# Performance work log

Hardware: AMD Instinct MI355X
Metric: run time of the kernel (lower is better)

Reference implementation:

```python
import jax, jax.numpy as jnp
import numpy as np

DIM = 512
HEADS = 8
DIM_HEAD = DIM // 8          # 64
M_LAND = DIM // 2            # 256 landmarks
PINV_ITERS = 6
KS = 33                      # residual depthwise conv kernel
EPS = 1e-8
LN_EPS = 1e-5


def setup_inputs() -> dict:
    key = jax.random.key(0)
    ks = jax.random.split(key, 5)
    b, n = 2, 8192
    inner = HEADS * DIM_HEAD
    x = jax.random.normal(ks[0], (b, n, DIM), jnp.float32)
    mask = jnp.ones((b, n), jnp.bool_)
    w_qkv = jax.random.normal(ks[1], (DIM, 3 * inner), jnp.float32) / np.sqrt(DIM)
    w_out = jax.random.normal(ks[2], (inner, DIM), jnp.float32) / np.sqrt(inner)
    b_out = jnp.zeros((DIM,), jnp.float32)
    conv_w = jax.random.normal(ks[3], (HEADS, 1, KS, 1), jnp.float32) / np.sqrt(KS)
    ln_w = jnp.ones((DIM,), jnp.float32)
    ln_b = jnp.zeros((DIM,), jnp.float32)
    return dict(x=x, mask=mask, ln_w=ln_w, ln_b=ln_b,
                w_qkv=w_qkv, w_out=w_out, b_out=b_out, conv_w=conv_w)


def _moore_penrose_pinv(x, iters):
    # lucidrains iterative pinv: z0 = x^T / (max(col_sums) * max(row_sums))
    abs_x = jnp.abs(x)
    col = abs_x.sum(-1)
    row = abs_x.sum(-2)
    z = jnp.swapaxes(x, -1, -2) / (jnp.max(col) * jnp.max(row))
    I = jnp.eye(x.shape[-1], dtype=x.dtype)
    for _ in range(iters):
        xz = x @ z
        z = 0.25 * z @ (13 * I - xz @ (15 * I - xz @ (7 * I - xz)))
    return z


def reference(x, mask, ln_w, ln_b, w_qkv, w_out, b_out, conv_w):
    b, n, _ = x.shape
    # LayerNorm (pre-norm)
    mu = x.mean(-1, keepdims=True)
    var = ((x - mu) ** 2).mean(-1, keepdims=True)
    xn = (x - mu) / jnp.sqrt(var + LN_EPS) * ln_w + ln_b
    # front-pad seq to multiple of num_landmarks (static; no-op when divisible)
    pad = (M_LAND - n % M_LAND) % M_LAND
    if pad:
        xn = jnp.pad(xn, ((0, 0), (pad, 0), (0, 0)))
        mask = jnp.pad(mask, ((0, 0), (pad, 0)), constant_values=False)
    N = n + pad
    qkv = xn @ w_qkv
    q, k, v = jnp.split(qkv, 3, axis=-1)
    rs = lambda t: t.reshape(b, N, HEADS, DIM_HEAD).transpose(0, 2, 1, 3)  # b h N d
    q, k, v = rs(q), rs(k), rs(v)
    m3 = mask[:, None, :]                       # b 1 N
    mf = m3[..., None].astype(q.dtype)
    q, k, v = q * mf, k * mf, v * mf
    q = q * (DIM_HEAD ** -0.5)
    l = N // M_LAND                             # tokens per landmark
    ql = q.reshape(b, HEADS, M_LAND, l, DIM_HEAD).sum(3)
    kl = k.reshape(b, HEADS, M_LAND, l, DIM_HEAD).sum(3)
    m_land_sum = m3.astype(q.dtype).reshape(b, 1, M_LAND, l).sum(-1)   # b 1 M
    divisor = m_land_sum[..., None] + EPS
    ql = ql / divisor
    kl = kl / divisor
    m_land = m_land_sum > 0                     # b 1 M
    sim1 = jnp.einsum('bhid,bhjd->bhij', q, kl)    # b h N M
    sim2 = jnp.einsum('bhid,bhjd->bhij', ql, kl)   # b h M M
    sim3 = jnp.einsum('bhid,bhjd->bhij', ql, k)    # b h M N
    NEG = -jnp.finfo(q.dtype).max
    sim1 = jnp.where(m3[..., None] & m_land[..., None, :], sim1, NEG)
    sim2 = jnp.where(m_land[..., None] & m_land[..., None, :], sim2, NEG)
    sim3 = jnp.where(m_land[..., None] & m3[..., None, :], sim3, NEG)
    a1 = jax.nn.softmax(sim1, -1)
    a2 = jax.nn.softmax(sim2, -1)
    a3 = jax.nn.softmax(sim3, -1)
    a2_inv = _moore_penrose_pinv(a2, PINV_ITERS)
    out = (a1 @ a2_inv) @ (a3 @ v)              # b h N d
    # residual depthwise conv over sequence dim (per head)
    res = jax.lax.conv_general_dilated(
        v, conv_w, window_strides=(1, 1),
        padding=((KS // 2, KS // 2), (0, 0)),
        dimension_numbers=('NCHW', 'OIHW', 'NCHW'),
        feature_group_count=HEADS)
    out = out + res
    out = out.transpose(0, 2, 1, 3).reshape(b, N, HEADS * DIM_HEAD)
    out = out @ w_out + b_out                   # dropout is identity at eval
    out = out[:, -n:]
    return x + out
```

## Files before the change

### kernel.cpp

```cpp
#include <hip/hip_runtime.h>


typedef __attribute__((ext_vector_type(8))) short bf16x8;
typedef __attribute__((ext_vector_type(4))) float f32x4;

static __device__ __forceinline__ ushort f2bf(float f) {
  union { float f; unsigned u; } c; c.f = f;
  const unsigned r = c.u + 0x7fffu + ((c.u >> 16) & 1u);
  return (ushort)(r >> 16);
}
static __device__ __forceinline__ float bf2f(ushort u) {
  union { unsigned u; float f; } c; c.u = ((unsigned)u) << 16;
  return c.f;
}

typedef __attribute__((address_space(1))) const unsigned int guint;
typedef __attribute__((address_space(3))) unsigned int luint;
static __device__ __forceinline__ void gload_lds16(const void* g, void* l) {
  __builtin_amdgcn_global_load_lds((guint*)g, (luint*)l, 16, 0, 0);
}

__global__ __launch_bounds__(256) void ln_kernel(const float* __restrict__ x,
                                                 const float* __restrict__ w,
                                                 const float* __restrict__ b,
                                                 ushort* __restrict__ xn) {
  const int row = blockIdx.x;
  const int t = threadIdx.x;
  const float* xr = x + (long long)row * 512;
  float v0 = xr[t], v1 = xr[t + 256];
  __shared__ float red[8];
  float s = v0 + v1;
#pragma unroll
  for (int o = 32; o; o >>= 1) s += __shfl_xor(s, o);
  if ((t & 63) == 0) red[t >> 6] = s;
  __syncthreads();
  const float mu = (red[0] + red[1] + red[2] + red[3]) * (1.0f / 512.0f);
  const float d0 = v0 - mu, d1 = v1 - mu;
  float qs = d0 * d0 + d1 * d1;
#pragma unroll
  for (int o = 32; o; o >>= 1) qs += __shfl_xor(qs, o);
  if ((t & 63) == 0) red[4 + (t >> 6)] = qs;
  __syncthreads();
  const float var = (red[4] + red[5] + red[6] + red[7]) * (1.0f / 512.0f);
  const float rs = rsqrtf(var + 1e-5f);
  ushort* xo = xn + (long long)row * 512;
  xo[t] = f2bf(d0 * rs * w[t] + b[t]);
  xo[t + 256] = f2bf(d1 * rs * w[t + 256] + b[t + 256]);
}

__global__ __launch_bounds__(256) void convert_T_bf16(const float* __restrict__ in,
                                                      ushort* __restrict__ out,
                                                      int R, int Cc) {
  const long long i = (long long)blockIdx.x * 256 + threadIdx.x;
  if (i >= (long long)R * Cc) return;
  const int c = (int)(i / R), r = (int)(i % R);
  out[i] = f2bf(in[(long long)r * Cc + c]);
}

__global__ __launch_bounds__(256) void gemm_bf16(
    const ushort* __restrict__ A, const ushort* __restrict__ Bt,
    float* __restrict__ C, ushort* __restrict__ uq, ushort* __restrict__ uk,
    ushort* __restrict__ uv,
    const float* __restrict__ bias, const float* __restrict__ xres,
    int K, int mode) {
  const int tid = threadIdx.x;
  const int wave = tid >> 6, lane = tid & 63;
  const int quad = lane >> 4, l16 = lane & 15;

  const int gx = gridDim.x;
  const int nwg = gx * gridDim.y;
  const int hid = blockIdx.y * gx + blockIdx.x;
  const int wid = (hid & 7) * (nwg >> 3) + (hid >> 3);
  const int tm = (wid / gx) * 128, tn = (wid % gx) * 128;

  const int wr = (wave >> 1) * 64, wc = (wave & 1) * 64;
  __shared__ __align__(16) ushort As[128 * 32];
  __shared__ __align__(16) ushort Bs[128 * 32];

  f32x4 acc[4][4];
#pragma unroll
  for (int i = 0; i < 4; ++i)
#pragma unroll
    for (int j = 0; j < 4; ++j) acc[i][j] = (f32x4)0.f;

  const int r0 = tid >> 2;
  const int c0 = (tid & 3) * 8;
  const ushort* gA0 = A + (long long)(tm + r0) * K + c0;
  const ushort* gA1 = A + (long long)(tm + 64 + r0) * K + c0;
  const ushort* gB0 = Bt + (long long)(tn + r0) * K + c0;
  const ushort* gB1 = Bt + (long long)(tn + 64 + r0) * K + c0;
  ushort* lA0 = As + (wave * 64) * 8;
  ushort* lA1 = As + (256 + wave * 64) * 8;
  ushort* lB0 = Bs + (wave * 64) * 8;
  ushort* lB1 = Bs + (256 + wave * 64) * 8;

  for (int kb = 0; kb < K; kb += 32) {
    __syncthreads();
    gload_lds16(gA0 + kb, lA0);
    gload_lds16(gA1 + kb, lA1);
    gload_lds16(gB0 + kb, lB0);
    gload_lds16(gB1 + kb, lB1);
    __syncthreads();
    bf16x8 af[4], bfr[4];
#pragma unroll
    for (int t = 0; t < 4; ++t) {
      af[t] = *(const bf16x8*)&As[(wr + t * 16 + l16) * 32 + quad * 8];
      bfr[t] = *(const bf16x8*)&Bs[(wc + t * 16 + l16) * 32 + quad * 8];
    }
#pragma unroll
    for (int i = 0; i < 4; ++i)
#pragma unroll
      for (int j = 0; j < 4; ++j)
        acc[i][j] = __builtin_amdgcn_mfma_f32_16x16x32_bf16(af[i], bfr[j], acc[i][j], 0, 0, 0);
  }

  if (mode == 2) {
#pragma unroll
    for (int ti = 0; ti < 4; ++ti) {
#pragma unroll
      for (int r = 0; r < 4; ++r) {
        const int gr = tm + wr + ti * 16 + quad * 4 + r;
        const int bb = gr >> 13, nn = gr & 8191;
#pragma unroll
        for (int tj = 0; tj < 4; ++tj) {
          const int gc = tn + wc + tj * 16 + l16;
          const int part = gc >> 9, hh = (gc >> 6) & 7, dd = gc & 63;
          float val = acc[ti][tj][r];
          if (part == 0) val *= 0.125f;
          ushort* dst = (part == 0) ? uq : ((part == 1) ? uk : uv);
          dst[((((long long)(bb * 8 + hh)) << 13) + nn) * 64 + dd] = f2bf(val);
        }
      }
    }
  } else {
#pragma unroll
    for (int ti = 0; ti < 4; ++ti) {
#pragma unroll
      for (int r = 0; r < 4; ++r) {
        const long long gr = tm + wr + ti * 16 + quad * 4 + r;
#pragma unroll
        for (int tj = 0; tj < 4; ++tj) {
          const int gc = tn + wc + tj * 16 + l16;
          const long long idx = gr * 512 + gc;
          C[idx] = acc[ti][tj][r] + bias[gc] + xres[idx];
        }
      }
    }
  }
}

__global__ __launch_bounds__(256) void gemm_f32(
    const float* __restrict__ A, const float* __restrict__ B,
    float* __restrict__ C, int K, int lda, int ldb, int ldc,
    long long sA, long long sB, long long sC) {
  const int tid = threadIdx.x;
  const int batch = blockIdx.z;
  A += (long long)batch * sA;
  B += (long long)batch * sB;
  C += (long long)batch * sC;
  const int tm = blockIdx.y * 64;
  const int tn = blockIdx.x * 64;

  __shared__ float As[16][65];
  __shared__ float Bs[16][65];

  const int tx = tid & 15, ty = tid >> 4;
  const int ar = tid >> 2, ac = (tid & 3) * 4;
  const int br = tid >> 4, bc = (tid & 15) * 4;

  float acc[4][4];
#pragma unroll
  for (int i = 0; i < 4; ++i)
#pragma unroll
    for (int j = 0; j < 4; ++j) acc[i][j] = 0.f;

  for (int kb = 0; kb < K; kb += 16) {
    const float4 a4 = *(const float4*)(A + (long long)(tm + ar) * lda + kb + ac);
    const float4 b4 = *(const float4*)(B + (long long)(kb + br) * ldb + tn + bc);
    __syncthreads();
    As[ac + 0][ar] = a4.x; As[ac + 1][ar] = a4.y;
    As[ac + 2][ar] = a4.z; As[ac + 3][ar] = a4.w;
    Bs[br][bc + 0] = b4.x; Bs[br][bc + 1] = b4.y;
    Bs[br][bc + 2] = b4.z; Bs[br][bc + 3] = b4.w;
    __syncthreads();
#pragma unroll
    for (int kk = 0; kk < 16; ++kk) {
      float av[4], bv[4];
#pragma unroll
      for (int i = 0; i < 4; ++i) av[i] = As[kk][ty * 4 + i];
#pragma unroll
      for (int j = 0; j < 4; ++j) bv[j] = Bs[kk][tx * 4 + j];
#pragma unroll
      for (int i = 0; i < 4; ++i)
#pragma unroll
        for (int j = 0; j < 4; ++j) acc[i][j] = fmaf(av[i], bv[j], acc[i][j]);
    }
  }
#pragma unroll
  for (int i = 0; i < 4; ++i) {
    const long long r = tm + ty * 4 + i;
#pragma unroll
    for (int j = 0; j < 4; ++j) C[r * ldc + tn + tx * 4 + j] = acc[i][j];
  }
}

static __device__ __forceinline__ void stage_body(
    int tc, int tr, int bh,
    const ushort* __restrict__ Ah, const ushort* __restrict__ Al,
    const ushort* __restrict__ BTh, const ushort* __restrict__ BTl,
    const ushort* __restrict__ D1h, const ushort* __restrict__ D1l,
    const ushort* __restrict__ D2h, const ushort* __restrict__ D2l,
    ushort* __restrict__ Ch, ushort* __restrict__ Cl,
    ushort* __restrict__ CTh, ushort* __restrict__ CTl,
    float alpha, float beta1, float beta2,
    long long sBT, long long sC, int ldc,
    ushort (*TBh)[36], ushort (*TBl)[36]) {
  const int tid = threadIdx.x;
  const int wave = tid >> 6, lane = tid & 63;
  const int quad = lane >> 4, l16 = lane & 15;
  const bool hasAl = (Al != nullptr);
  const bool hasBl = (BTl != nullptr);

  const ushort* A_h = Ah + (long long)bh * 65536 + (long long)(tr + wave * 16 + l16) * 256;
  const ushort* A_l = (hasAl ? Al : Ah) + (long long)bh * 65536 +
                      (long long)(tr + wave * 16 + l16) * 256;
  const ushort* B_h0 = BTh + (long long)bh * sBT + (long long)(tc + l16) * 256;
  const ushort* B_l0 = (hasBl ? BTl : BTh) + (long long)bh * sBT +
                       (long long)(tc + l16) * 256;

  f32x4 acc[2];
  acc[0] = (f32x4)0.f; acc[1] = (f32x4)0.f;

#pragma unroll
  for (int kc = 0; kc < 8; ++kc) {
    const int ko = kc * 32 + quad * 8;
    const bf16x8 a_h = *(const bf16x8*)(A_h + ko);
    bf16x8 a_l;
    if (hasAl) a_l = *(const bf16x8*)(A_l + ko);
#pragma unroll
    for (int ct = 0; ct < 2; ++ct) {
      const bf16x8 b_h = *(const bf16x8*)(B_h0 + ct * 4096 + ko);
      acc[ct] = __builtin_amdgcn_mfma_f32_16x16x32_bf16(a_h, b_h, acc[ct], 0, 0, 0);
      if (hasBl) {
        const bf16x8 b_l = *(const bf16x8*)(B_l0 + ct * 4096 + ko);
        acc[ct] = __builtin_amdgcn_mfma_f32_16x16x32_bf16(a_h, b_l, acc[ct], 0, 0, 0);
      }
      if (hasAl)
        acc[ct] = __builtin_amdgcn_mfma_f32_16x16x32_bf16(a_l, b_h, acc[ct], 0, 0, 0);
    }
  }

#pragma unroll
  for (int ct = 0; ct < 2; ++ct) {
#pragma unroll
    for (int r = 0; r < 4; ++r) {
      const int rl = wave * 16 + quad * 4 + r;
      const int clc = ct * 16 + l16;
      float val = alpha * acc[ct][r];
      if (D1h) {
        const long long di = (long long)bh * 65536 + (long long)(tr + rl) * 256 + tc + clc;
        float d = bf2f(D1h[di]);
        if (D1l) d += bf2f(D1l[di]);
        val += beta1 * d;
      }
      if (D2h) {
        const long long di = (long long)bh * 65536 + (long long)(tr + rl) * 256 + tc + clc;
        float d = bf2f(D2h[di]);
        if (D2l) d += bf2f(D2l[di]);
        val += beta2 * d;
      }
      const ushort h = f2bf(val);
      TBh[rl][clc] = h;
      TBl[rl][clc] = f2bf(val - bf2f(h));
    }
  }
  __syncthreads();
  if (Ch) {
    const int rl = tid >> 2, seg = (tid & 3) * 8;
    const long long ci = (long long)bh * sC + (long long)(tr + rl) * ldc + tc + seg;
    *(uint4*)&Ch[ci] = *(const uint4*)&TBh[rl][seg];
    if (Cl) *(uint4*)&Cl[ci] = *(const uint4*)&TBl[rl][seg];
  }
  if (CTh) {
    const int clc = tid >> 3, seg = (tid & 7) * 8;
    union { uint4 u; ushort s[8]; } th, tl;
#pragma unroll
    for (int j = 0; j < 8; ++j) {
      th.s[j] = TBh[seg + j][clc];
      tl.s[j] = TBl[seg + j][clc];
    }
    const long long gi = (long long)bh * 65536 + (long long)(tc + clc) * 256 + tr + seg;
    *(uint4*)&CTh[gi] = th.u;
    if (CTl) *(uint4*)&CTl[gi] = tl.u;
  }
}

__global__ __launch_bounds__(256) void gemm_split(
    const ushort* __restrict__ Ah, const ushort* __restrict__ Al,
    const ushort* __restrict__ BTh, const ushort* __restrict__ BTl,
    const ushort* __restrict__ D1h, const ushort* __restrict__ D1l,
    const ushort* __restrict__ D2h, const ushort* __restrict__ D2l,
    ushort* __restrict__ Ch, ushort* __restrict__ Cl,
    ushort* __restrict__ CTh, ushort* __restrict__ CTl,
    float alpha, float beta1, float beta2,
    long long sBT, long long sC, int ldc) {
  __shared__ ushort TBh[64][36];
  __shared__ ushort TBl[64][36];
  stage_body(blockIdx.x * 32, blockIdx.y * 64, blockIdx.z,
             Ah, Al, BTh, BTl, D1h, D1l, D2h, D2l, Ch, Cl, CTh, CTl,
             alpha, beta1, beta2, sBT, sC, ldc, TBh, TBl);
}

__global__ __launch_bounds__(256) void gemm_dual(
    const ushort* __restrict__ zA, const ushort* __restrict__ yA,
    const ushort* __restrict__ BT,
    ushort* __restrict__ zC, ushort* __restrict__ zCT,
    ushort* __restrict__ yC, ushort* __restrict__ yCT) {
  __shared__ ushort TBh[64][36];
  __shared__ ushort TBl[64][36];
  const int by = blockIdx.y;
  if (by < 4)
    stage_body(blockIdx.x * 32, by * 64, blockIdx.z,
               zA, nullptr, BT, nullptr, zA, nullptr, nullptr, nullptr,
               zC, nullptr, zCT, nullptr, -0.25f, 3.25f, 0.f,
               65536, 65536, 256, TBh, TBl);
  else
    stage_body(blockIdx.x * 32, (by - 4) * 64, blockIdx.z,
               yA, nullptr, BT, nullptr, yA, nullptr, nullptr, nullptr,
               yC, nullptr, yCT, nullptr, -0.25f, 3.25f, 0.f,
               65536, 65536, 256, TBh, TBl);
}

__global__ __launch_bounds__(64) void landmark_kernel(
    const ushort* __restrict__ q, const ushort* __restrict__ k,
    float* __restrict__ qlf, float* __restrict__ klTf,
    ushort* __restrict__ qlb, ushort* __restrict__ klb) {
  const int bh = blockIdx.y, i = blockIdx.x, d = threadIdx.x;
  const long long base = (((long long)bh << 13) + i * 32) * 64 + d;
  float sq = 0.f, sk = 0.f;
#pragma unroll
  for (int j = 0; j < 32; ++j) {
    sq += bf2f(q[base + j * 64]);
    sk += bf2f(k[base + j * 64]);
  }
  const float mq = sq * (1.0f / 32.0f), mk = sk * (1.0f / 32.0f);
  qlf[((long long)bh * 256 + i) * 64 + d] = mq;
  klTf[((long long)bh * 64 + d) * 256 + i] = mk;
  qlb[((long long)bh * 256 + i) * 64 + d] = f2bf(mq);
  klb[((long long)bh * 256 + i) * 64 + d] = f2bf(mk);
}

__global__ __launch_bounds__(256) void softmax256(float* __restrict__ a) {
  const long long row = (long long)blockIdx.x * 4 + (threadIdx.x >> 6);
  const int lane = threadIdx.x & 63;
  float* p = a + row * 256 + lane * 4;
  float4 vv = *(float4*)p;
  float m = fmaxf(fmaxf(vv.x, vv.y), fmaxf(vv.z, vv.w));
#pragma unroll
  for (int o = 32; o; o >>= 1) m = fmaxf(m, __shfl_xor(m, o));
  vv.x = __expf(vv.x - m); vv.y = __expf(vv.y - m);
  vv.z = __expf(vv.z - m); vv.w = __expf(vv.w - m);
  float s = vv.x + vv.y + vv.z + vv.w;
#pragma unroll
  for (int o = 32; o; o >>= 1) s += __shfl_xor(s, o);
  const float inv = 1.0f / s;
  vv.x *= inv; vv.y *= inv; vv.z *= inv; vv.w *= inv;
  *(float4*)p = vv;
}

__global__ __launch_bounds__(256) void flash_mfma(
    const ushort* __restrict__ Q, const ushort* __restrict__ K,
    const ushort* __restrict__ V, float* __restrict__ Out,
    const ushort* __restrict__ CV,
    float* __restrict__ Opart, float* __restrict__ Mpart,
    float* __restrict__ Lpart,
    long long sQ, long long sK, long long sV, long long sO,
    int iters, int nsplit) {
  const int bh = blockIdx.z, mt = blockIdx.y, ns = blockIdx.x;
  const int tid = threadIdx.x;
  const int wave = tid >> 6, lane = tid & 63;
  const int quad = lane >> 4, l16 = lane & 15;
  __shared__ ushort Vt[64][72];
  __shared__ ushort Ps[64][72];

  const ushort* Qb = Q + (long long)bh * sQ + (long long)(mt * 64) * 64;
  const ushort* Kb = K + (long long)bh * sK + (long long)(ns * iters * 64) * 64;
  const ushort* Vb = V + (long long)bh * sV + (long long)(ns * iters * 64) * 64;

  bf16x8 aq[2];
#pragma unroll
  for (int kc = 0; kc < 2; ++kc)
    aq[kc] = *(const bf16x8*)(Qb + (long long)(wave * 16 + l16) * 64 + kc * 32 + quad * 8);

  f32x4 acc[4];
  float mrow[4], lrow[4];
#pragma unroll
  for (int dt = 0; dt < 4; ++dt) acc[dt] = (f32x4)0.f;
#pragma unroll
  for (int r = 0; r < 4; ++r) { mrow[r] = -1e30f; lrow[r] = 0.f; }

  for (int it = 0; it < iters; ++it) {
    __syncthreads();
    for (int i = tid; i < 512; i += 256) {
      const int key = i & 63, c8 = (i >> 6) * 8;
      union { uint4 u; ushort s[8]; } t;
      t.u = *(const uint4*)(Vb + (long long)(it * 64 + key) * 64 + c8);
#pragma unroll
      for (int j = 0; j < 8; ++j) Vt[c8 + j][key] = t.s[j];
    }
    f32x4 sfr[4];
#pragma unroll
    for (int kt = 0; kt < 4; ++kt) {
      sfr[kt] = (f32x4)0.f;
#pragma unroll
      for (int kc = 0; kc < 2; ++kc) {
        const bf16x8 bk = *(const bf16x8*)(Kb +
            (long long)(it * 64 + kt * 16 + l16) * 64 + kc * 32 + quad * 8);
        sfr[kt] = __builtin_amdgcn_mfma_f32_16x16x32_bf16(aq[kc], bk, sfr[kt], 0, 0, 0);
      }
    }
#pragma unroll
    for (int r = 0; r < 4; ++r) {
      float rm = fmaxf(fmaxf(sfr[0][r], sfr[1][r]), fmaxf(sfr[2][r], sfr[3][r]));
#pragma unroll
      for (int off = 1; off < 16; off <<= 1) rm = fmaxf(rm, __shfl_xor(rm, off));
      const float mn = fmaxf(mrow[r], rm);
      const float scv = __expf(mrow[r] - mn);
      float rs = 0.f;
#pragma unroll
      for (int kt = 0; kt < 4; ++kt) {
        const float p = __expf(sfr[kt][r] - mn);
        sfr[kt][r] = p;
        rs += p;
      }
#pragma unroll
      for (int off = 1; off < 16; off <<= 1) rs += __shfl_xor(rs, off);
      lrow[r] = lrow[r] * scv + rs;
      mrow[r] = mn;
#pragma unroll
      for (int dt = 0; dt < 4; ++dt) acc[dt][r] *= scv;
#pragma unroll
      for (int kt = 0; kt < 4; ++kt)
        Ps[wave * 16 + quad * 4 + r][kt * 16 + l16] = f2bf(sfr[kt][r]);
    }
    __syncthreads();
#pragma unroll
    for (int kc = 0; kc < 2; ++kc) {
      const bf16x8 ap = *(const bf16x8*)&Ps[wave * 16 + l16][kc * 32 + quad * 8];
#pragma unroll
      for (int dt = 0; dt < 4; ++dt) {
        const bf16x8 bv = *(const bf16x8*)&Vt[dt * 16 + l16][kc * 32 + quad * 8];
        acc[dt] = __builtin_amdgcn_mfma_f32_16x16x32_bf16(ap, bv, acc[dt], 0, 0, 0);
      }
    }
  }

  if (nsplit == 1) {
    if (CV) {
      const int b = bh >> 3, h = bh & 7;
      const ushort* cvb = CV + (((long long)bh << 13) + mt * 64) * 64;
      ushort* Ob = (ushort*)Out + ((long long)(b * 8192 + mt * 64)) * 512 + h * 64;
#pragma unroll
      for (int r = 0; r < 4; ++r) {
        const float inv = 1.0f / lrow[r];
        const int row = wave * 16 + quad * 4 + r;
#pragma unroll
        for (int dt = 0; dt < 4; ++dt) {
          const int col = dt * 16 + l16;
          const float val = acc[dt][r] * inv + bf2f(cvb[(long long)row * 64 + col]);
          Ob[(long long)row * 512 + col] = f2bf(val);
        }
      }
    } else {
      ushort* Ob = (ushort*)Out + (long long)bh * sO + (long long)(mt * 64) * 64;
#pragma unroll
      for (int r = 0; r < 4; ++r) {
        const float inv = 1.0f / lrow[r];
        const int row = wave * 16 + quad * 4 + r;
#pragma unroll
        for (int dt = 0; dt < 4; ++dt)
          Ob[(long long)row * 64 + dt * 16 + l16] = f2bf(acc[dt][r] * inv);
      }
    }
  } else {
    const long long pbase = ((long long)(bh * gridDim.y + mt) * nsplit + ns);
    const int row0 = wave * 16 + quad * 4;
#pragma unroll
    for (int r = 0; r < 4; ++r) {
#pragma unroll
      for (int dt = 0; dt < 4; ++dt)
        Opart[(pbase * 64 + row0 + r) * 64 + dt * 16 + l16] = acc[dt][r];
      if (l16 == 0) {
        Mpart[pbase * 64 + row0 + r] = mrow[r];
        Lpart[pbase * 64 + row0 + r] = lrow[r];
      }
    }
  }
}

__global__ __launch_bounds__(256) void flash_merge(
    const float* __restrict__ Opart, const float* __restrict__ Mpart,
    const float* __restrict__ Lpart, ushort* __restrict__ a3vTh,
    ushort* __restrict__ a3vTl, int nsplit) {
  const int bm = blockIdx.x >> 4;
  const int rg = blockIdx.x & 15;
  const int bh = bm >> 2, mt = bm & 3;
  const int c = threadIdx.x & 63, rb = threadIdx.x >> 6;
  const int r = rg * 4 + rb;
  float ms = -1e30f;
  for (int ns = 0; ns < nsplit; ++ns)
    ms = fmaxf(ms, Mpart[(bm * nsplit + ns) * 64 + r]);
  float L = 0.f, O = 0.f;
  for (int ns = 0; ns < nsplit; ++ns) {
    const float w = __expf(Mpart[(bm * nsplit + ns) * 64 + r] - ms);
    L += w * Lpart[(bm * nsplit + ns) * 64 + r];
    O += w * Opart[((long long)(bm * nsplit + ns) * 64 + r) * 64 + c];
  }
  const float val = O / L;
  const ushort h = f2bf(val);
  const long long ti = (long long)bh * 16384 + (long long)c * 256 + mt * 64 + r;
  a3vTh[ti] = h;
  a3vTl[ti] = f2bf(val - bf2f(h));
}

__global__ void pm_init(float* __restrict__ pm) {
  if (threadIdx.x < 2) pm[threadIdx.x] = 0.f;
}

__global__ __launch_bounds__(256) void a2_sums(const float* __restrict__ a2,
                                               float* __restrict__ pm) {
  const int p = blockIdx.x, bh = blockIdx.y;
  const float* m = a2 + (long long)bh * 65536;
  const int tid = threadIdx.x;
  __shared__ float red[4];
  {
    const int r = p * 32 + (tid >> 3);
    const int c0 = (tid & 7) * 32;
    float s = 0.f;
#pragma unroll 8
    for (int j = 0; j < 32; ++j) s += m[r * 256 + c0 + j];
    s += __shfl_xor(s, 1); s += __shfl_xor(s, 2); s += __shfl_xor(s, 4);
    float mx = s;
#pragma unroll
    for (int o = 8; o < 64; o <<= 1) mx = fmaxf(mx, __shfl_xor(mx, o));
    if ((tid & 63) == 0) red[tid >> 6] = mx;
    __syncthreads();
    if (tid == 0) {
      mx = fmaxf(fmaxf(red[0], red[1]), fmaxf(red[2], red[3]));
      atomicMax((int*)&pm[0], __float_as_int(mx));
    }
    __syncthreads();
  }
  {
    const int c = p * 32 + (tid >> 3);
    const int r0 = (tid & 7) * 32;
    float s = 0.f;
#pragma unroll 8
    for (int j = 0; j < 32; ++j) s += m[(r0 + j) * 256 + c];
    s += __shfl_xor(s, 1); s += __shfl_xor(s, 2); s += __shfl_xor(s, 4);
    float mx = s;
#pragma unroll
    for (int o = 8; o < 64; o <<= 1) mx = fmaxf(mx, __shfl_xor(mx, o));
    if ((tid & 63) == 0) red[tid >> 6] = mx;
    __syncthreads();
    if (tid == 0) {
      mx = fmaxf(fmaxf(red[0], red[1]), fmaxf(red[2], red[3]));
      atomicMax((int*)&pm[1], __float_as_int(mx));
    }
  }
}

__global__ __launch_bounds__(256) void pinv_init(
    const float* __restrict__ a2, const float* __restrict__ pm,
    ushort* __restrict__ a2h, ushort* __restrict__ a2l,
    ushort* __restrict__ zh, ushort* __restrict__ zTh) {
  const int bh = blockIdx.y;
  const float s = 1.0f / (pm[0] * pm[1]);
  const long long base = (long long)bh * 65536;
  const int i0 = blockIdx.x * 4096;
  for (int t = threadIdx.x; t < 4096; t += 256) {
    const int idx = i0 + t;
    const float v = a2[base + idx];
    const ushort h = f2bf(v);
    a2h[base + idx] = h;
    a2l[base + idx] = f2bf(v - bf2f(h));
    zTh[base + idx] = f2bf(v * s);
    const float vt = a2[base + ((long long)(idx & 255) << 8) + (idx >> 8)] * s;
    zh[base + idx] = f2bf(vt);
  }
}

__global__ __launch_bounds__(256) void conv_store(const ushort* __restrict__ v,
                                                  const float* __restrict__ w,
                                                  ushort* __restrict__ cv) {
  const int bh = blockIdx.y;
  const int n0 = blockIdx.x * 128;
  const int h = bh & 7;
  __shared__ float vs[160][64];
  __shared__ float ws[33];
  if (threadIdx.x < 33) ws[threadIdx.x] = w[h * 33 + threadIdx.x];
  for (int i = threadIdx.x; i < 160 * 8; i += 256) {
    const int r = i >> 3, c8 = (i & 7) * 8;
    const int n = n0 - 16 + r;
    if (n >= 0 && n < 8192) {
      union { uint4 u; ushort s[8]; } t;
      t.u = *(const uint4*)(v + (((long long)bh << 13) + n) * 64 + c8);
#pragma unroll
      for (int j = 0; j < 8; ++j) vs[r][c8 + j] = bf2f(t.s[j]);
    } else {
#pragma unroll
      for (int j = 0; j < 8; ++j) vs[r][c8 + j] = 0.f;
    }
  }
  __syncthreads();
  const int d = threadIdx.x & 63, r0 = threadIdx.x >> 6;
  for (int rr = r0; rr < 128; rr += 4) {
    float acc = 0.f;
#pragma unroll
    for (int kk = 0; kk < 33; ++kk) acc += ws[kk] * vs[rr + kk][d];
    cv[(((long long)bh << 13) + n0 + rr) * 64 + d] = f2bf(acc);
  }
}

static inline void launch_split(hipStream_t st, int gridX,
    const ushort* Ah, const ushort* Al,
    const ushort* BTh, const ushort* BTl, long long sBT,
    const ushort* D1h, const ushort* D1l, float beta1,
    const ushort* D2h, const ushort* D2l, float beta2,
    ushort* Ch, ushort* Cl, ushort* CTh, ushort* CTl,
    long long sC, int ldc, float alpha) {
  dim3 grid((unsigned)gridX, 4, 16);
  hipLaunchKernelGGL(gemm_split, grid, dim3(256), 0, st, Ah, Al, BTh, BTl,
                     D1h, D1l, D2h, D2l, Ch, Cl, CTh, CTl,
                     alpha, beta1, beta2, sBT, sC, ldc);
}

extern "C" void kernel_launch(void* const* d_in, const int* in_sizes, int n_in,
                              void* d_out, int out_size, void* d_ws, size_t ws_size,
                              hipStream_t stream) {
  const float* x = (const float*)d_in[0];
  const float* ln_w = (const float*)d_in[2];
  const float* ln_b = (const float*)d_in[3];
  const float* w_qkv = (const float*)d_in[4];
  const float* w_out = (const float*)d_in[5];
  const float* b_out = (const float*)d_in[6];
  const float* conv_w = (const float*)d_in[7];
  float* out = (float*)d_out;

  float* ws = (float*)d_ws;
  float* R = ws;
  float* a2   = R + 10485760LL;
  float* qlf  = a2 + 1048576LL;
  float* klTf = qlf + 262144LL;
  float* pm   = klTf + 262144LL;
  ushort* q_bf   = (ushort*)(pm + 64);
  ushort* k_bf   = q_bf + 8388608LL;
  ushort* v_bf   = k_bf + 8388608LL;
  ushort* xn_bf  = v_bf + 8388608LL;
  ushort* ql_bf  = xn_bf + 8388608LL;
  ushort* kl_bf  = ql_bf + 262144LL;
  ushort* tb_bf  = kl_bf + 262144LL;
  ushort* wqT_bf = tb_bf + 262144LL;
  ushort* woT_bf = wqT_bf + 786432LL;
  ushort* a2h    = woT_bf + 262144LL;
  ushort* a2l    = a2h + 1048576LL;
  ushort* a3vTh  = a2l + 1048576LL;
  ushort* a3vTl  = a3vTh + 262144LL;

  float* Opart = R;
  float* Mpart = R + 4194304LL;
  float* Lpart = R + 4194304LL + 65536;
  ushort* cb = (ushort*)R;
  ushort* zah = cb;                ushort* zal = cb + 1048576LL;
  ushort* zaTh = cb + 2097152LL;
  ushort* zbh = cb + 4194304LL;
  ushort* zbTh = cb + 6291456LL;
  ushort* Ph = cb + 8388608LL;     ushort* Pl = cb + 9437184LL;
  ushort* PTh = cb + 10485760LL;   ushort* PTl = cb + 11534336LL;
  ushort* P2h = cb + 12582912LL;   ushort* P2l = cb + 13631488LL;
  ushort* P2Th = cb + 14680064LL;  ushort* P2Tl = cb + 15728640LL;
  ushort* T2Th = cb + 18874368LL;  ushort* T2Tl = cb + 19922944LL;
  ushort* Yah = Pl;    ushort* YaTh = PTl;
  ushort* Ybh = P2l;   ushort* YbTh = P2Tl;
  ushort* ao2_bf = (ushort*)R;
  ushort* cv_bf  = (ushort*)R + 8388608LL;

  hipLaunchKernelGGL(convert_T_bf16, dim3(3072), dim3(256), 0, stream,
                     w_qkv, wqT_bf, 512, 1536);
  hipLaunchKernelGGL(convert_T_bf16, dim3(1024), dim3(256), 0, stream,
                     w_out, woT_bf, 512, 512);
  hipLaunchKernelGGL(ln_kernel, dim3(16384), dim3(256), 0, stream, x, ln_w, ln_b, xn_bf);
  hipLaunchKernelGGL(gemm_bf16, dim3(12, 128), dim3(256), 0, stream,
                     xn_bf, wqT_bf, nullptr, q_bf, k_bf, v_bf, nullptr, nullptr, 512, 2);
  hipLaunchKernelGGL(landmark_kernel, dim3(256, 16), dim3(64), 0, stream,
                     q_bf, k_bf, qlf, klTf, ql_bf, kl_bf);
  {
    dim3 g(4, 4, 16);
    hipLaunchKernelGGL(gemm_f32, g, dim3(256), 0, stream, qlf, klTf, a2,
                       64, 64, 256, 256, 16384LL, 16384LL, 65536LL);
  }
  hipLaunchKernelGGL(softmax256, dim3(1024), dim3(256), 0, stream, a2);
  hipLaunchKernelGGL(flash_mfma, dim3(16, 4, 16), dim3(256), 0, stream,
                     ql_bf, k_bf, v_bf, (float*)nullptr, (const ushort*)nullptr,
                     Opart, Mpart, Lpart,
                     16384LL, 524288LL, 524288LL, 0LL, 8, 16);
  hipLaunchKernelGGL(flash_merge, dim3(1024), dim3(256), 0, stream,
                     Opart, Mpart, Lpart, a3vTh, a3vTl, 16);
  hipLaunchKernelGGL(pm_init, dim3(1), dim3(64), 0, stream, pm);
  hipLaunchKernelGGL(a2_sums, dim3(8, 16), dim3(256), 0, stream, a2, pm);
  hipLaunchKernelGGL(pinv_init, dim3(16, 16), dim3(256), 0, stream, a2, pm,
                     a2h, a2l, zah, zaTh);
  launch_split(stream, 8, a2h, nullptr, zaTh, nullptr, 65536,
               nullptr, nullptr, 0.f, nullptr, nullptr, 0.f,
               Yah, nullptr, YaTh, nullptr, 65536, 256, 1.f);
  {
    ushort *zh = zah, *zTh = zaTh, *zwh = zbh, *zwTh = zbTh;
    ushort *Yh = Yah, *YTh = YaTh, *Ywh = Ybh, *YwTh = YbTh;
    for (int it = 0; it < 5; ++it) {
      launch_split(stream, 8, Yh, nullptr, YTh, nullptr, 65536,
                   nullptr, nullptr, 0.f, nullptr, nullptr, 0.f,
                   P2h, nullptr, P2Th, nullptr, 65536, 256, 1.f);
      launch_split(stream, 8, Yh, nullptr, P2Th, nullptr, 65536,
                   Yh, nullptr, 15.f, P2h, nullptr, -7.f,
                   nullptr, nullptr, T2Th, nullptr, 65536, 256, 1.f);
      if (it < 4) {
        hipLaunchKernelGGL(gemm_dual, dim3(8, 8, 16), dim3(256), 0, stream,
                           zh, Yh, T2Th, zwh, zwTh, Ywh, YwTh);
        ushort* t;
        t = zh; zh = zwh; zwh = t;  t = zTh; zTh = zwTh; zwTh = t;
        t = Yh; Yh = Ywh; Ywh = t;  t = YTh; YTh = YwTh; YwTh = t;
      } else {
        launch_split(stream, 8, zh, nullptr, T2Th, nullptr, 65536,
                     zh, nullptr, 3.25f, nullptr, nullptr, 0.f,
                     zwh, nullptr, zwTh, nullptr, 65536, 256, -0.25f);
      }
    }
  }
  launch_split(stream, 8, a2h, a2l, zbTh, nullptr, 65536,
               nullptr, nullptr, 0.f, nullptr, nullptr, 0.f,
               Ph, Pl, PTh, PTl, 65536, 256, 1.f);
  launch_split(stream, 8, Ph, Pl, PTh, PTl, 65536,
               nullptr, nullptr, 0.f, nullptr, nullptr, 0.f,
               P2h, P2l, P2Th, P2Tl, 65536, 256, 1.f);
  launch_split(stream, 8, Ph, Pl, P2Th, P2Tl, 65536,
               Ph, Pl, 15.f, P2h, P2l, -7.f,
               nullptr, nullptr, T2Th, T2Tl, 65536, 256, 1.f);
  launch_split(stream, 8, zbh, nullptr, T2Th, T2Tl, 65536,
               zbh, nullptr, 3.25f, nullptr, nullptr, 0.f,
               zah, zal, nullptr, nullptr, 65536, 256, -0.25f);
  launch_split(stream, 2, zah, zal, a3vTh, a3vTl, 16384,
               nullptr, nullptr, 0.f, nullptr, nullptr, 0.f,
               tb_bf, nullptr, nullptr, nullptr, 16384, 64, 1.f);
  hipLaunchKernelGGL(conv_store, dim3(64, 16), dim3(256), 0, stream, v_bf, conv_w, cv_bf);
  hipLaunchKernelGGL(flash_mfma, dim3(1, 128, 16), dim3(256), 0, stream,
                     q_bf, kl_bf, tb_bf, (float*)ao2_bf, cv_bf,
                     (float*)nullptr, (float*)nullptr, (float*)nullptr,
                     524288LL, 16384LL, 16384LL, 0LL, 4, 1);
  hipLaunchKernelGGL(gemm_bf16, dim3(4, 128), dim3(256), 0, stream,
                     ao2_bf, woT_bf, out, nullptr, nullptr, nullptr, b_out, x, 512, 3);
}
```

Before: 605.9 us.

## Store QKV projection row-major and read heads via strided access

The QKV GEMM epilogue now writes its output as one row-major [b*n, 1536] buffer instead of scattering into per-head q/k/v tensors. The landmark, conv and flash kernels take batch, head and row strides so they can read heads directly from this interleaved layout. The aim is to make the GEMM stores contiguous and drop the per-element head/part address arithmetic. In exchange, the downstream kernels read with a 1536-element row stride, which may hurt their coalescing and cache locality.

```diff
diff --git a/kernel.cpp b/kernel.cpp
--- a/kernel.cpp
+++ b/kernel.cpp
@@ -59,8 +59,7 @@
 
 __global__ __launch_bounds__(256) void gemm_bf16(
     const ushort* __restrict__ A, const ushort* __restrict__ Bt,
-    float* __restrict__ C, ushort* __restrict__ uq, ushort* __restrict__ uk,
-    ushort* __restrict__ uv,
+    float* __restrict__ C, ushort* __restrict__ uq,
     const float* __restrict__ bias, const float* __restrict__ xres,
     int K, int mode) {
   const int tid = threadIdx.x;
@@ -115,21 +114,16 @@
   }
 
   if (mode == 2) {
+    const float scale = ((tn + wc) >> 9) == 0 ? 0.125f : 1.0f;
 #pragma unroll
     for (int ti = 0; ti < 4; ++ti) {
 #pragma unroll
       for (int r = 0; r < 4; ++r) {
         const int gr = tm + wr + ti * 16 + quad * 4 + r;
-        const int bb = gr >> 13, nn = gr & 8191;
-#pragma unroll
-        for (int tj = 0; tj < 4; ++tj) {
-          const int gc = tn + wc + tj * 16 + l16;
-          const int part = gc >> 9, hh = (gc >> 6) & 7, dd = gc & 63;
-          float val = acc[ti][tj][r];
-          if (part == 0) val *= 0.125f;
-          ushort* dst = (part == 0) ? uq : ((part == 1) ? uk : uv);
-          dst[((((long long)(bb * 8 + hh)) << 13) + nn) * 64 + dd] = f2bf(val);
-        }
+        ushort* drow = uq + (long long)gr * 1536 + tn + wc;
+#pragma unroll
+        for (int tj = 0; tj < 4; ++tj)
+          drow[tj * 16 + l16] = f2bf(acc[ti][tj][r] * scale);
       }
     }
   } else {
@@ -332,16 +326,17 @@
 }
 
 __global__ __launch_bounds__(64) void landmark_kernel(
-    const ushort* __restrict__ q, const ushort* __restrict__ k,
+    const ushort* __restrict__ qkv,
     float* __restrict__ qlf, float* __restrict__ klTf,
     ushort* __restrict__ qlb, ushort* __restrict__ klb) {
   const int bh = blockIdx.y, i = blockIdx.x, d = threadIdx.x;
-  const long long base = (((long long)bh << 13) + i * 32) * 64 + d;
+  const int b = bh >> 3, h = bh & 7;
+  const long long rowbase = ((long long)(b * 8192 + i * 32)) * 1536 + h * 64 + d;
   float sq = 0.f, sk = 0.f;
 #pragma unroll
   for (int j = 0; j < 32; ++j) {
-    sq += bf2f(q[base + j * 64]);
-    sk += bf2f(k[base + j * 64]);
+    sq += bf2f(qkv[rowbase + (long long)j * 1536]);
+    sk += bf2f(qkv[rowbase + (long long)j * 1536 + 512]);
   }
   const float mq = sq * (1.0f / 32.0f), mk = sk * (1.0f / 32.0f);
   qlf[((long long)bh * 256 + i) * 64 + d] = mq;
@@ -374,8 +369,10 @@
     const ushort* __restrict__ CV,
     float* __restrict__ Opart, float* __restrict__ Mpart,
     float* __restrict__ Lpart,
-    long long sQ, long long sK, long long sV, long long sO,
-    int iters, int nsplit) {
+    long long sQ, long long hQ, int rQ,
+    long long sK, long long hK, int rK,
+    long long sV, long long hV, int rV,
+    long long sO, int iters, int nsplit) {
   const int bh = blockIdx.z, mt = blockIdx.y, ns = blockIdx.x;
   const int tid = threadIdx.x;
   const int wave = tid >> 6, lane = tid & 63;
@@ -383,14 +380,14 @@
   __shared__ ushort Vt[64][72];
   __shared__ ushort Ps[64][72];
 
-  const ushort* Qb = Q + (long long)bh * sQ + (long long)(mt * 64) * 64;
-  const ushort* Kb = K + (long long)bh * sK + (long long)(ns * iters * 64) * 64;
-  const ushort* Vb = V + (long long)bh * sV + (long long)(ns * iters * 64) * 64;
+  const ushort* Qb = Q + (bh >> 3) * sQ + (bh & 7) * hQ + (long long)(mt * 64) * rQ;
+  const ushort* Kb = K + (bh >> 3) * sK + (bh & 7) * hK + (long long)(ns * iters * 64) * rK;
+  const ushort* Vb = V + (bh >> 3) * sV + (bh & 7) * hV + (long long)(ns * iters * 64) * rV;
 
   bf16x8 aq[2];
 #pragma unroll
   for (int kc = 0; kc < 2; ++kc)
-    aq[kc] = *(const bf16x8*)(Qb + (long long)(wave * 16 + l16) * 64 + kc * 32 + quad * 8);
+    aq[kc] = *(const bf16x8*)(Qb + (long long)(wave * 16 + l16) * rQ + kc * 32 + quad * 8);
 
   f32x4 acc[4];
   float mrow[4], lrow[4];
@@ -404,7 +401,7 @@
     for (int i = tid; i < 512; i += 256) {
       const int key = i & 63, c8 = (i >> 6) * 8;
       union { uint4 u; ushort s[8]; } t;
-      t.u = *(const uint4*)(Vb + (long long)(it * 64 + key) * 64 + c8);
+      t.u = *(const uint4*)(Vb + (long long)(it * 64 + key) * rV + c8);
 #pragma unroll
       for (int j = 0; j < 8; ++j) Vt[c8 + j][key] = t.s[j];
     }
@@ -415,7 +412,7 @@
 #pragma unroll
       for (int kc = 0; kc < 2; ++kc) {
         const bf16x8 bk = *(const bf16x8*)(Kb +
-            (long long)(it * 64 + kt * 16 + l16) * 64 + kc * 32 + quad * 8);
+            (long long)(it * 64 + kt * 16 + l16) * rK + kc * 32 + quad * 8);
         sfr[kt] = __builtin_amdgcn_mfma_f32_16x16x32_bf16(aq[kc], bk, sfr[kt], 0, 0, 0);
       }
     }
@@ -590,12 +587,12 @@
   }
 }
 
-__global__ __launch_bounds__(256) void conv_store(const ushort* __restrict__ v,
+__global__ __launch_bounds__(256) void conv_store(const ushort* __restrict__ qkv,
                                                   const float* __restrict__ w,
                                                   ushort* __restrict__ cv) {
   const int bh = blockIdx.y;
   const int n0 = blockIdx.x * 128;
-  const int h = bh & 7;
+  const int b = bh >> 3, h = bh & 7;
   __shared__ float vs[160][64];
   __shared__ float ws[33];
   if (threadIdx.x < 33) ws[threadIdx.x] = w[h * 33 + threadIdx.x];
@@ -604,7 +601,7 @@
     const int n = n0 - 16 + r;
     if (n >= 0 && n < 8192) {
       union { uint4 u; ushort s[8]; } t;
-      t.u = *(const uint4*)(v + (((long long)bh << 13) + n) * 64 + c8);
+      t.u = *(const uint4*)(qkv + ((long long)(b * 8192 + n)) * 1536 + 1024 + h * 64 + c8);
 #pragma unroll
       for (int j = 0; j < 8; ++j) vs[r][c8 + j] = bf2f(t.s[j]);
     } else {
@@ -653,10 +650,8 @@
   float* qlf  = a2 + 1048576LL;
   float* klTf = qlf + 262144LL;
   float* pm   = klTf + 262144LL;
-  ushort* q_bf   = (ushort*)(pm + 64);
-  ushort* k_bf   = q_bf + 8388608LL;
-  ushort* v_bf   = k_bf + 8388608LL;
-  ushort* xn_bf  = v_bf + 8388608LL;
+  ushort* qkv_bf = (ushort*)(pm + 64);
+  ushort* xn_bf  = qkv_bf + 25165824LL;
   ushort* ql_bf  = xn_bf + 8388608LL;
   ushort* kl_bf  = ql_bf + 262144LL;
   ushort* tb_bf  = kl_bf + 262144LL;
@@ -685,15 +680,22 @@
   ushort* ao2_bf = (ushort*)R;
   ushort* cv_bf  = (ushort*)R + 8388608LL;
 
+  const long long QKV_S = 12582912LL;
+  const long long QKV_H = 64LL;
+  const int QKV_R = 1536;
+  const long long CPT_S = 131072LL;
+  const long long CPT_H = 16384LL;
+  const int CPT_R = 64;
+
   hipLaunchKernelGGL(convert_T_bf16, dim3(3072), dim3(256), 0, stream,
                      w_qkv, wqT_bf, 512, 1536);
   hipLaunchKernelGGL(convert_T_bf16, dim3(1024), dim3(256), 0, stream,
                      w_out, woT_bf, 512, 512);
   hipLaunchKernelGGL(ln_kernel, dim3(16384), dim3(256), 0, stream, x, ln_w, ln_b, xn_bf);
   hipLaunchKernelGGL(gemm_bf16, dim3(12, 128), dim3(256), 0, stream,
-                     xn_bf, wqT_bf, nullptr, q_bf, k_bf, v_bf, nullptr, nullptr, 512, 2);
+                     xn_bf, wqT_bf, nullptr, qkv_bf, nullptr, nullptr, 512, 2);
   hipLaunchKernelGGL(landmark_kernel, dim3(256, 16), dim3(64), 0, stream,
-                     q_bf, k_bf, qlf, klTf, ql_bf, kl_bf);
+                     qkv_bf, qlf, klTf, ql_bf, kl_bf);
   {
     dim3 g(4, 4, 16);
     hipLaunchKernelGGL(gemm_f32, g, dim3(256), 0, stream, qlf, klTf, a2,
@@ -701,9 +703,12 @@
   }
   hipLaunchKernelGGL(softmax256, dim3(1024), dim3(256), 0, stream, a2);
   hipLaunchKernelGGL(flash_mfma, dim3(16, 4, 16), dim3(256), 0, stream,
-                     ql_bf, k_bf, v_bf, (float*)nullptr, (const ushort*)nullptr,
-                     Opart, Mpart, Lpart,
-                     16384LL, 524288LL, 524288LL, 0LL, 8, 16);
+                     ql_bf, qkv_bf + 512, qkv_bf + 1024, (float*)nullptr,
+                     (const ushort*)nullptr, Opart, Mpart, Lpart,
+                     CPT_S, CPT_H, CPT_R,
+                     QKV_S, QKV_H, QKV_R,
+                     QKV_S, QKV_H, QKV_R,
+                     0LL, 8, 16);
   hipLaunchKernelGGL(flash_merge, dim3(1024), dim3(256), 0, stream,
                      Opart, Mpart, Lpart, a3vTh, a3vTl, 16);
   hipLaunchKernelGGL(pm_init, dim3(1), dim3(64), 0, stream, pm);
@@ -751,11 +756,15 @@
   launch_split(stream, 2, zah, zal, a3vTh, a3vTl, 16384,
                nullptr, nullptr, 0.f, nullptr, nullptr, 0.f,
                tb_bf, nullptr, nullptr, nullptr, 16384, 64, 1.f);
-  hipLaunchKernelGGL(conv_store, dim3(64, 16), dim3(256), 0, stream, v_bf, conv_w, cv_bf);
+  hipLaunchKernelGGL(conv_store, dim3(64, 16), dim3(256), 0, stream,
+                     qkv_bf, conv_w, cv_bf);
   hipLaunchKernelGGL(flash_mfma, dim3(1, 128, 16), dim3(256), 0, stream,
-                     q_bf, kl_bf, tb_bf, (float*)ao2_bf, cv_bf,
+                     qkv_bf, kl_bf, tb_bf, (float*)ao2_bf, cv_bf,
                      (float*)nullptr, (float*)nullptr, (float*)nullptr,
-                     524288LL, 16384LL, 16384LL, 0LL, 4, 1);
+                     QKV_S, QKV_H, QKV_R,
+                     CPT_S, CPT_H, CPT_R,
+                     CPT_S, CPT_H, CPT_R,
+                     0LL, 4, 1);
   hipLaunchKernelGGL(gemm_bf16, dim3(4, 128), dim3(256), 0, stream,
-                     ao2_bf, woT_bf, out, nullptr, nullptr, nullptr, b_out, x, 512, 3);
-}
+                     ao2_bf, woT_bf, out, nullptr, b_out, x, 512, 3);
+}
```

Result: no change. 617.0 us (+1.8%).
